# Performance work log

Hardware: AMD Instinct MI355X
Metric: run time of the kernel (lower is better)

The kernel has to match this reference:

```python
import jax, jax.numpy as jnp
import numpy as np

N_NODES = 50000
N_EDGES = 800000
F_IN = 128
F_OUT = 128
EPS_STD = 1e-5  # PyG StdAggregation epsilon


def setup_inputs() -> dict:
    key = jax.random.key(0)
    ks = jax.random.split(key, 8)
    x = jax.random.normal(ks[0], (N_NODES, F_IN), dtype=jnp.float32)
    edge_index = jax.random.randint(ks[1], (2, N_EDGES), 0, N_NODES, dtype=jnp.int64)
    s = 0.02
    # pre_nn: Linear(2*F_IN -> F_IN)
    W_pre = jax.random.normal(ks[2], (2 * F_IN, F_IN), dtype=jnp.float32) * s
    b_pre = jnp.zeros((F_IN,), dtype=jnp.float32)
    # post_nn: Linear((1 + 4 aggregators * 1 scaler) * F_IN -> F_OUT)
    W_post = jax.random.normal(ks[3], (5 * F_IN, F_OUT), dtype=jnp.float32) * s
    b_post = jnp.zeros((F_OUT,), dtype=jnp.float32)
    # final lin: Linear(F_OUT -> F_OUT)
    W_lin = jax.random.normal(ks[4], (F_OUT, F_OUT), dtype=jnp.float32) * s
    b_lin = jnp.zeros((F_OUT,), dtype=jnp.float32)
    return {"x": x, "W_pre": W_pre, "b_pre": b_pre, "W_post": W_post,
            "b_post": b_post, "W_lin": W_lin, "b_lin": b_lin,
            "edge_index": edge_index}


def _pna_forward(x, W_pre, b_pre, W_post, b_post, W_lin, b_lin, edge_index):
    N = x.shape[0]
    src = edge_index[0]  # x_j (source / neighbor)
    dst = edge_index[1]  # x_i (target / aggregation index)

    # per-edge message: Linear(cat(x_i, x_j))  [E, F_IN]
    h = jnp.concatenate([x[dst], x[src]], axis=-1) @ W_pre + b_pre

    ones = jnp.ones((h.shape[0],), dtype=h.dtype)
    deg = jax.ops.segment_sum(ones, dst, num_segments=N)          # in-degree [N]
    deg_c = jnp.maximum(deg, 1.0)[:, None]

    s1 = jax.ops.segment_sum(h, dst, num_segments=N)
    s2 = jax.ops.segment_sum(h * h, dst, num_segments=N)
    mean = s1 / deg_c
    var = jax.nn.relu(s2 / deg_c - mean * mean)
    std = jnp.sqrt(var + EPS_STD)

    has_nb = (deg > 0)[:, None]
    mx = jax.ops.segment_max(h, dst, num_segments=N)
    mn = jax.ops.segment_min(h, dst, num_segments=N)
    mx = jnp.where(has_nb, mx, 0.0)
    mn = jnp.where(has_nb, mn, 0.0)

    # aggregators in declared order: mean, max, min, std -> [N, 4*F_IN]
    agg = jnp.concatenate([mean, mx, mn, std], axis=-1)

    # 'linear' degree scaler: deg / avg_deg
    avg_deg = jnp.mean(deg)
    agg = agg * (deg[:, None] / avg_deg)

    out = jnp.concatenate([x, agg], axis=-1) @ W_post + b_post
    out = out @ W_lin + b_lin
    return jax.nn.relu(out)


def reference(x, W_pre, b_pre, W_post, b_post, W_lin, b_lin, edge_index):
    return _pna_forward(x, W_pre, b_pre, W_post, b_post, W_lin, b_lin, edge_index)
```

## Files before the change

kernel.cpp:

```cpp
#include <hip/hip_runtime.h>
#include <hip/hip_bf16.h>
#include <math.h>


typedef _Float16 f16;
typedef _Float16 f16x8 __attribute__((ext_vector_type(8)));
typedef _Float16 f16x2 __attribute__((ext_vector_type(2)));
typedef float    f32x4 __attribute__((ext_vector_type(4)));

__device__ __forceinline__ unsigned packh2(float a, float b) {
  union { unsigned u; f16x2 h; } x; x.h = (f16x2){(f16)a, (f16)b}; return x.u;
}
__device__ __forceinline__ float2 unpackh2(unsigned v) {
  union { unsigned u; f16x2 h; } x; x.u = v;
  return make_float2((float)x.h.x, (float)x.h.y);
}

template<int KTOT, int KO1, bool HASB, bool RELU, bool OUTF16>
__global__ __launch_bounds__(256) void gemm_reg_k(
    const f16* __restrict__ A1, const f16* __restrict__ A2,
    const f16* __restrict__ Wt, const float* __restrict__ bias,
    float* __restrict__ outF, f16* __restrict__ outH, int M, int ldOut)
{
  const int tid = threadIdx.x;
  const int l   = tid & 63;
  const int w   = tid >> 6;
  const int wr  = (w >> 1) * 32;
  const int wc  = (w & 1) * 64;
  const int li  = l & 15, kg = l >> 4;
  const int rowBase = blockIdx.x * 64;
  const int colBase = blockIdx.y * 128;
  constexpr int ld2 = (KTOT > KO1) ? (KTOT - KO1) : 1;

  int aOff[2], a2Off[2], bOff[4];
#pragma unroll
  for (int r = 0; r < 2; ++r) {
    int gr = rowBase + wr + r * 16 + li; if (gr > M - 1) gr = M - 1;
    aOff[r] = gr * KO1; a2Off[r] = gr * ld2;
  }
#pragma unroll
  for (int c = 0; c < 4; ++c) bOff[c] = (colBase + wc + c * 16 + li) * KTOT;

  f32x4 acc[2][4];
#pragma unroll
  for (int r = 0; r < 2; ++r)
#pragma unroll
    for (int c = 0; c < 4; ++c) acc[r][c] = (f32x4){0.f, 0.f, 0.f, 0.f};

  f16x8 aA[2], bA[4], aB[2], bB[4];
  auto lf = [&](int k0, f16x8 a[2], f16x8 b[4]) {
    int k = k0 + kg * 8;
    if (KO1 == KTOT || k0 < KO1) {
#pragma unroll
      for (int r = 0; r < 2; ++r) a[r] = *reinterpret_cast<const f16x8*>(A1 + aOff[r] + k);
    } else {
#pragma unroll
      for (int r = 0; r < 2; ++r) a[r] = *reinterpret_cast<const f16x8*>(A2 + a2Off[r] + (k - KO1));
    }
#pragma unroll
    for (int c = 0; c < 4; ++c) b[c] = *reinterpret_cast<const f16x8*>(Wt + bOff[c] + k);
  };

  lf(0, aA, bA);
  for (int k0 = 0; k0 < KTOT; k0 += 64) {
    lf(k0 + 32, aB, bB);
#pragma unroll
    for (int r = 0; r < 2; ++r)
#pragma unroll
      for (int c = 0; c < 4; ++c)
        acc[r][c] = __builtin_amdgcn_mfma_f32_16x16x32_f16(aA[r], bA[c], acc[r][c], 0, 0, 0);
    if (k0 + 64 < KTOT) lf(k0 + 64, aA, bA);
#pragma unroll
    for (int r = 0; r < 2; ++r)
#pragma unroll
      for (int c = 0; c < 4; ++c)
        acc[r][c] = __builtin_amdgcn_mfma_f32_16x16x32_f16(aB[r], bB[c], acc[r][c], 0, 0, 0);
  }

  float bv[4];
#pragma unroll
  for (int c = 0; c < 4; ++c) {
    int col = colBase + wc + c * 16 + li;
    bv[c] = (HASB && col < 128) ? bias[col] : 0.f;
  }

  if constexpr (OUTF16) {
    __shared__ __align__(16) f16 Ls[64][136];
#pragma unroll
    for (int c = 0; c < 4; ++c) {
      int col = wc + c * 16 + li;
#pragma unroll
      for (int r = 0; r < 2; ++r)
#pragma unroll
        for (int j = 0; j < 4; ++j) {
          float v = acc[r][c][j] + bv[c];
          if (RELU) v = fmaxf(v, 0.f);
          Ls[wr + r * 16 + kg * 4 + j][col] = (f16)v;
        }
    }
    __syncthreads();
#pragma unroll
    for (int i = 0; i < 4; ++i) {
      int s = tid + 256 * i;
      int rr = s >> 4, cc = (s & 15) * 8;
      int gr = rowBase + rr;
      if (gr < M)
        *reinterpret_cast<float4*>(&outH[(size_t)gr * ldOut + colBase + cc]) =
            *reinterpret_cast<const float4*>(&Ls[rr][cc]);
    }
  } else {
    __shared__ __align__(16) float Lf[64][132];
#pragma unroll
    for (int c = 0; c < 4; ++c) {
      int col = wc + c * 16 + li;
#pragma unroll
      for (int r = 0; r < 2; ++r)
#pragma unroll
        for (int j = 0; j < 4; ++j) {
          float v = acc[r][c][j] + bv[c];
          if (RELU) v = fmaxf(v, 0.f);
          Lf[wr + r * 16 + kg * 4 + j][col] = v;
        }
    }
    __syncthreads();
#pragma unroll
    for (int i = 0; i < 8; ++i) {
      int s = tid + 256 * i;
      int rr = s >> 5, cc = (s & 31) * 4;
      int gr = rowBase + rr;
      if (gr < M)
        *reinterpret_cast<float4*>(&outF[(size_t)gr * ldOut + colBase + cc]) =
            *reinterpret_cast<const float4*>(&Lf[rr][cc]);
    }
  }
}

__global__ void cvt_x_k(const float* __restrict__ x, f16* __restrict__ xf, int n) {
  int i = (blockIdx.x * 256 + threadIdx.x) * 4;
  if (i < n) {
    float4 v = *reinterpret_cast<const float4*>(&x[i]);
    xf[i] = (f16)v.x; xf[i + 1] = (f16)v.y; xf[i + 2] = (f16)v.z; xf[i + 3] = (f16)v.w;
  }
}

__global__ void prep_wpre_k(const float* __restrict__ W, f16* __restrict__ Wt) {
  int e = blockIdx.x * 256 + threadIdx.x;
  if (e < 256 * 128) {
    int n = e >> 7, k = e & 127;
    float v = (n < 128) ? W[(size_t)k * 128 + n] : W[(size_t)(128 + k) * 128 + (n - 128)];
    Wt[e] = (f16)v;
  }
}

__global__ void fold_w_k(const float* __restrict__ Wpost, const float* __restrict__ bpost,
                         const float* __restrict__ Wlin,  const float* __restrict__ blin,
                         f16* __restrict__ WtComb, float* __restrict__ bcomb) {
  int e = blockIdx.x * 256 + threadIdx.x;
  if (e < 640 * 128) {
    int n = e / 640, k = e - n * 640;
    float s = 0.f;
#pragma unroll 4
    for (int m = 0; m < 128; ++m) s += Wpost[(size_t)k * 128 + m] * Wlin[(size_t)m * 128 + n];
    WtComb[(size_t)n * 640 + k] = (f16)s;
  } else if (e < 640 * 128 + 128) {
    int n = e - 640 * 128;
    float s = blin[n];
#pragma unroll 4
    for (int m = 0; m < 128; ++m) s += bpost[m] * Wlin[(size_t)m * 128 + n];
    bcomb[n] = s;
  }
}

__global__ void zero_k(int* __restrict__ p, int n) {
  int i = blockIdx.x * 256 + threadIdx.x;
  if (i < n) p[i] = 0;
}

__global__ void count_k(const int* __restrict__ ei, int* __restrict__ deg, int E) {
  int e = blockIdx.x * 256 + threadIdx.x;
  if (e < E) atomicAdd(&deg[ei[E + e]], 1);
}

__device__ __forceinline__ int blockExclScan(int v, int* wtot) {
  int lane = threadIdx.x & 63, wid = threadIdx.x >> 6;
  int x = v;
#pragma unroll
  for (int d = 1; d < 64; d <<= 1) {
    int y = __shfl_up(x, d);
    if (lane >= d) x += y;
  }
  if (lane == 63) wtot[wid] = x;
  __syncthreads();
  if (threadIdx.x == 0) {
    int s = 0;
#pragma unroll
    for (int k = 0; k < 4; ++k) { int t = wtot[k]; wtot[k] = s; s += t; }
  }
  __syncthreads();
  return wtot[wid] + x - v;
}

__global__ __launch_bounds__(256) void scan1_k(const int* __restrict__ deg,
                                               int* __restrict__ offs,
                                               int* __restrict__ partials, int n) {
  __shared__ int wtot[4];
  int i = blockIdx.x * 256 + threadIdx.x;
  int v = (i < n) ? deg[i] : 0;
  int e = blockExclScan(v, wtot);
  if (i < n) offs[i] = e;
  if (threadIdx.x == 255) partials[blockIdx.x] = e + v;
}

__global__ __launch_bounds__(256) void scan2_k(int* __restrict__ partials, int nb) {
  __shared__ int wtot[4];
  int v = (threadIdx.x < nb) ? partials[threadIdx.x] : 0;
  int e = blockExclScan(v, wtot);
  if (threadIdx.x < nb) partials[threadIdx.x] = e;
}

__global__ void scan3_k(const int* __restrict__ partials, int* __restrict__ offs,
                        int* __restrict__ cur, int n, int E) {
  int i = blockIdx.x * 256 + threadIdx.x;
  if (i < n) {
    int v = offs[i] + partials[i >> 8];
    offs[i] = v; cur[i] = v;
  }
  if (i == 0) offs[n] = E;
}

__global__ void scatter_k(const int* __restrict__ ei, int* __restrict__ cursor,
                          int* __restrict__ ssrc, int E) {
  int e = blockIdx.x * 256 + threadIdx.x;
  if (e < E) {
    int d = ei[E + e];
    int pos = atomicAdd(&cursor[d], 1);
    ssrc[pos] = ei[e];
  }
}

__global__ __launch_bounds__(256) void agg_k(
    const f16* __restrict__ CP, const int* __restrict__ offs,
    const int* __restrict__ ssrc, f16* __restrict__ AGG, int N)
{
  int w = threadIdx.x >> 6;
  int t = threadIdx.x & 63;
  int i = blockIdx.x * 4 + w;
  if (i >= N) return;
  int start = offs[i], end = offs[i + 1];
  int deg = end - start;
  unsigned* AGGu = (unsigned*)AGG;
  size_t o = (size_t)i * 256 + t;
  if (deg == 0) {
    AGGu[o] = 0u; AGGu[o + 64] = 0u; AGGu[o + 128] = 0u; AGGu[o + 192] = 0u;
    return;
  }
  const unsigned* CPu = (const unsigned*)CP;
  float s0 = 0.f, s1 = 0.f, q0 = 0.f, q1 = 0.f;
  float mx0 = -INFINITY, mx1 = -INFINITY, mn0 = INFINITY, mn1 = INFINITY;

  auto accum = [&](unsigned u) {
    float2 v = unpackh2(u);
    s0 += v.x; s1 += v.y;
    q0 = fmaf(v.x, v.x, q0); q1 = fmaf(v.y, v.y, q1);
    mx0 = fmaxf(mx0, v.x); mx1 = fmaxf(mx1, v.y);
    mn0 = fminf(mn0, v.x); mn1 = fminf(mn1, v.y);
  };

  for (int base = start; base < end; base += 64) {
    int cnt = min(end - base, 64);
    int myoff = 0;
    if (base + t < end) myoff = ssrc[base + t] * 128 + 64;
    int j = 0;
    for (; j + 4 <= cnt; j += 4) {
      int o0 = __shfl(myoff, j);
      int o1 = __shfl(myoff, j + 1);
      int o2 = __shfl(myoff, j + 2);
      int o3 = __shfl(myoff, j + 3);
      unsigned u0 = CPu[o0 + t];
      unsigned u1 = CPu[o1 + t];
      unsigned u2 = CPu[o2 + t];
      unsigned u3 = CPu[o3 + t];
      accum(u0); accum(u1); accum(u2); accum(u3);
    }
    for (; j < cnt; ++j) {
      int o0 = __shfl(myoff, j);
      accum(CPu[o0 + t]);
    }
  }

  float2 c = unpackh2(CPu[(size_t)i * 128 + t]);
  float degf = (float)deg;
  float inv = 1.f / degf;
  float m10 = s0 * inv, m11 = s1 * inv;
  float var0 = fmaxf(q0 * inv - m10 * m10, 0.f);
  float var1 = fmaxf(q1 * inv - m11 * m11, 0.f);
  float sd0 = sqrtf(var0 + 1e-5f), sd1 = sqrtf(var1 + 1e-5f);
  float sc = degf * (1.0f / 16.0f);
  AGGu[o]       = packh2((c.x + m10) * sc, (c.y + m11) * sc);
  AGGu[o + 64]  = packh2((c.x + mx0) * sc, (c.y + mx1) * sc);
  AGGu[o + 128] = packh2((c.x + mn0) * sc, (c.y + mn1) * sc);
  AGGu[o + 192] = packh2(sd0 * sc, sd1 * sc);
}

extern "C" void kernel_launch(void* const* d_in, const int* in_sizes, int n_in,
                              void* d_out, int out_size, void* d_ws, size_t ws_size,
                              hipStream_t stream) {
  const float* x      = (const float*)d_in[0];
  const float* W_pre  = (const float*)d_in[1];
  const float* b_pre  = (const float*)d_in[2];
  const float* W_post = (const float*)d_in[3];
  const float* b_post = (const float*)d_in[4];
  const float* W_lin  = (const float*)d_in[5];
  const float* b_lin  = (const float*)d_in[6];
  const int*   ei     = (const int*)d_in[7];

  const int N = in_sizes[0] / 128;
  const int E = in_sizes[7] / 2;

  char* ws = (char*)d_ws;
  size_t off = 0;
  auto alloc = [&](size_t bytes) -> void* {
    void* p = ws + off; off += (bytes + 255) & ~(size_t)255; return p;
  };
  f16*   xf     = (f16*)  alloc((size_t)N * 128 * 2);
  f16*   CP     = (f16*)  alloc((size_t)N * 256 * 2);
  f16*   AGG    = (f16*)  alloc((size_t)N * 512 * 2);
  f16*   WtPre  = (f16*)  alloc(256 * 128 * 2);
  f16*   WtComb = (f16*)  alloc(128 * 640 * 2);
  float* bcomb  = (float*)alloc(128 * 4);
  int*   ssrc   = (int*)  alloc((size_t)E * 4);
  int*   deg    = (int*)  alloc((size_t)N * 4);
  int*   offs   = (int*)  alloc((size_t)(N + 1) * 4);
  int*   cur    = (int*)  alloc((size_t)N * 4);
  int*   parts  = (int*)  alloc(1024 * 4);

  const int gTile = (N + 63) / 64;
  const int gE    = (E + 255) / 256;
  const int gN    = (N + 255) / 256;

  cvt_x_k<<<(N * 128 / 4 + 255) / 256, 256, 0, stream>>>(x, xf, N * 128);
  prep_wpre_k<<<(256 * 128 + 255) / 256, 256, 0, stream>>>(W_pre, WtPre);
  fold_w_k<<<(640 * 128 + 128 + 255) / 256, 256, 0, stream>>>(W_post, b_post, W_lin, b_lin, WtComb, bcomb);

  zero_k<<<gN, 256, 0, stream>>>(deg, N);

  gemm_reg_k<128, 128, true, false, true><<<dim3(gTile, 2), 256, 0, stream>>>(
      xf, nullptr, WtPre, b_pre, nullptr, CP, N, 256);

  count_k<<<gE, 256, 0, stream>>>(ei, deg, E);
  scan1_k<<<gN, 256, 0, stream>>>(deg, offs, parts, N);
  scan2_k<<<1, 256, 0, stream>>>(parts, gN);
  scan3_k<<<gN, 256, 0, stream>>>(parts, offs, cur, N, E);
  scatter_k<<<gE, 256, 0, stream>>>(ei, cur, ssrc, E);

  agg_k<<<(N + 3) / 4, 256, 0, stream>>>(CP, offs, ssrc, AGG, N);

  gemm_reg_k<640, 128, true, true, false><<<dim3(gTile, 1), 256, 0, stream>>>(
      xf, AGG, WtComb, bcomb, (float*)d_out, nullptr, N, 128);
}
```

Before: 312.7 us.

## Fuse neighbor aggregation with post-GEMM via LDS, merge setup kernels

```diff
diff --git a/kernel.cpp b/kernel.cpp
--- a/kernel.cpp
+++ b/kernel.cpp
@@ -7,6 +7,8 @@
 typedef _Float16 f16x8 __attribute__((ext_vector_type(8)));
 typedef _Float16 f16x2 __attribute__((ext_vector_type(2)));
 typedef float    f32x4 __attribute__((ext_vector_type(4)));
+
+#define NPB 32
 
 __device__ __forceinline__ unsigned packh2(float a, float b) {
   union { unsigned u; f16x2 h; } x; x.h = (f16x2){(f16)a, (f16)b}; return x.u;
@@ -135,6 +137,141 @@
   }
 }
 
+__global__ __launch_bounds__(256) void aggmm_k(
+    const f16* __restrict__ CP, const f16* __restrict__ xf,
+    const int* __restrict__ offs, const int* __restrict__ ssrc,
+    const f16* __restrict__ Wt, const float* __restrict__ bcomb,
+    float* __restrict__ out, int N)
+{
+  __shared__ __align__(16) char ldsbuf[NPB * 1024];
+  const int tid = threadIdx.x;
+  const int l = tid & 63, w = tid >> 6;
+  const int blockBase = blockIdx.x * NPB;
+  const unsigned* CPu = (const unsigned*)CP;
+
+  {
+    const int t = l;
+    for (int q = 0; q < NPB / 4; ++q) {
+      const int rloc = w * (NPB / 4) + q;
+      const int i = blockBase + rloc;
+      const unsigned sw = ((unsigned)(rloc & 15)) << 4;
+      int deg = 0, start = 0;
+      if (i < N) { start = offs[i]; deg = offs[i + 1] - start; }
+      if (deg == 0) {
+        *reinterpret_cast<unsigned*>(&ldsbuf[rloc * 1024 + (((t)       * 4) ^ sw)]) = 0u;
+        *reinterpret_cast<unsigned*>(&ldsbuf[rloc * 1024 + (((t + 64)  * 4) ^ sw)]) = 0u;
+        *reinterpret_cast<unsigned*>(&ldsbuf[rloc * 1024 + (((t + 128) * 4) ^ sw)]) = 0u;
+        *reinterpret_cast<unsigned*>(&ldsbuf[rloc * 1024 + (((t + 192) * 4) ^ sw)]) = 0u;
+        continue;
+      }
+      const int end = start + deg;
+      float s0 = 0.f, s1 = 0.f, q0 = 0.f, q1 = 0.f;
+      float mx0 = -INFINITY, mx1 = -INFINITY, mn0 = INFINITY, mn1 = INFINITY;
+      auto accum = [&](unsigned u) {
+        float2 v = unpackh2(u);
+        s0 += v.x; s1 += v.y;
+        q0 = fmaf(v.x, v.x, q0); q1 = fmaf(v.y, v.y, q1);
+        mx0 = fmaxf(mx0, v.x); mx1 = fmaxf(mx1, v.y);
+        mn0 = fminf(mn0, v.x); mn1 = fminf(mn1, v.y);
+      };
+      for (int base = start; base < end; base += 64) {
+        int cnt = min(end - base, 64);
+        int myoff = 0;
+        if (base + t < end) myoff = ssrc[base + t] * 128 + 64;
+        int j = 0;
+        for (; j + 4 <= cnt; j += 4) {
+          int o0 = __shfl(myoff, j);
+          int o1 = __shfl(myoff, j + 1);
+          int o2 = __shfl(myoff, j + 2);
+          int o3 = __shfl(myoff, j + 3);
+          unsigned u0 = CPu[o0 + t];
+          unsigned u1 = CPu[o1 + t];
+          unsigned u2 = CPu[o2 + t];
+          unsigned u3 = CPu[o3 + t];
+          accum(u0); accum(u1); accum(u2); accum(u3);
+        }
+        for (; j < cnt; ++j) accum(CPu[__shfl(myoff, j) + t]);
+      }
+      float2 c = unpackh2(CPu[(size_t)i * 128 + t]);
+      float degf = (float)deg;
+      float inv = 1.f / degf;
+      float m10 = s0 * inv, m11 = s1 * inv;
+      float var0 = fmaxf(q0 * inv - m10 * m10, 0.f);
+      float var1 = fmaxf(q1 * inv - m11 * m11, 0.f);
+      float sd0 = sqrtf(var0 + 1e-5f), sd1 = sqrtf(var1 + 1e-5f);
+      float sc = degf * (1.0f / 16.0f);
+      *reinterpret_cast<unsigned*>(&ldsbuf[rloc * 1024 + (((t)       * 4) ^ sw)]) = packh2((c.x + m10) * sc, (c.y + m11) * sc);
+      *reinterpret_cast<unsigned*>(&ldsbuf[rloc * 1024 + (((t + 64)  * 4) ^ sw)]) = packh2((c.x + mx0) * sc, (c.y + mx1) * sc);
+      *reinterpret_cast<unsigned*>(&ldsbuf[rloc * 1024 + (((t + 128) * 4) ^ sw)]) = packh2((c.x + mn0) * sc, (c.y + mn1) * sc);
+      *reinterpret_cast<unsigned*>(&ldsbuf[rloc * 1024 + (((t + 192) * 4) ^ sw)]) = packh2(sd0 * sc, sd1 * sc);
+    }
+  }
+  __syncthreads();
+
+  const int li = l & 15, kg = l >> 4;
+  const int wr = (w >> 1) * 16;
+  const int wc = (w & 1) * 64;
+  const int aRow = wr + li;
+  int grA = blockBase + aRow; if (grA > N - 1) grA = N - 1;
+  const int aOffG = grA * 128;
+  const unsigned swA = ((unsigned)(aRow & 15)) << 4;
+  int bOff[4];
+#pragma unroll
+  for (int c = 0; c < 4; ++c) bOff[c] = (wc + c * 16 + li) * 640;
+
+  f32x4 acc[4];
+#pragma unroll
+  for (int c = 0; c < 4; ++c) acc[c] = (f32x4){0.f, 0.f, 0.f, 0.f};
+
+  auto lf = [&](int k0, f16x8& a, f16x8 b[4]) {
+    int k = k0 + kg * 8;
+    if (k0 < 128) {
+      a = *reinterpret_cast<const f16x8*>(xf + aOffG + k);
+    } else {
+      unsigned bo = (unsigned)((k - 128) * 2);
+      a = *reinterpret_cast<const f16x8*>(&ldsbuf[aRow * 1024 + (bo ^ swA)]);
+    }
+#pragma unroll
+    for (int c = 0; c < 4; ++c) b[c] = *reinterpret_cast<const f16x8*>(Wt + bOff[c] + k);
+  };
+  auto mm = [&](f16x8 a, f16x8 b[4]) {
+#pragma unroll
+    for (int c = 0; c < 4; ++c)
+      acc[c] = __builtin_amdgcn_mfma_f32_16x16x32_f16(a, b[c], acc[c], 0, 0, 0);
+  };
+
+  f16x8 aA, bA[4], aB, bB[4];
+  lf(0, aA, bA);
+  for (int k0 = 0; k0 < 640; k0 += 64) {
+    lf(k0 + 32, aB, bB);
+    mm(aA, bA);
+    if (k0 + 64 < 640) lf(k0 + 64, aA, bA);
+    mm(aB, bB);
+  }
+
+  float bv[4];
+#pragma unroll
+  for (int c = 0; c < 4; ++c) bv[c] = bcomb[wc + c * 16 + li];
+
+  __syncthreads();
+  float* Lf = (float*)ldsbuf;
+#pragma unroll
+  for (int c = 0; c < 4; ++c)
+#pragma unroll
+    for (int j = 0; j < 4; ++j)
+      Lf[(wr + kg * 4 + j) * 132 + wc + c * 16 + li] = fmaxf(acc[c][j] + bv[c], 0.f);
+  __syncthreads();
+#pragma unroll
+  for (int i2 = 0; i2 < 4; ++i2) {
+    int s = tid + 256 * i2;
+    int rr = s >> 5, cc = (s & 31) * 4;
+    int gr = blockBase + rr;
+    if (gr < N)
+      *reinterpret_cast<float4*>(&out[(size_t)gr * 128 + cc]) =
+          *reinterpret_cast<const float4*>(&Lf[rr * 132 + cc]);
+  }
+}
+
 __global__ void cvt_x_k(const float* __restrict__ x, f16* __restrict__ xf, int n) {
   int i = (blockIdx.x * 256 + threadIdx.x) * 4;
   if (i < n) {
@@ -143,37 +280,33 @@
   }
 }
 
-__global__ void prep_wpre_k(const float* __restrict__ W, f16* __restrict__ Wt) {
+__global__ void setup_k(const float* __restrict__ Wpre,
+                        const float* __restrict__ Wpost, const float* __restrict__ bpost,
+                        const float* __restrict__ Wlin,  const float* __restrict__ blin,
+                        f16* __restrict__ WtPre, f16* __restrict__ WtComb,
+                        float* __restrict__ bcomb, int* __restrict__ deg, int N) {
   int e = blockIdx.x * 256 + threadIdx.x;
   if (e < 256 * 128) {
     int n = e >> 7, k = e & 127;
-    float v = (n < 128) ? W[(size_t)k * 128 + n] : W[(size_t)(128 + k) * 128 + (n - 128)];
-    Wt[e] = (f16)v;
-  }
-}
-
-__global__ void fold_w_k(const float* __restrict__ Wpost, const float* __restrict__ bpost,
-                         const float* __restrict__ Wlin,  const float* __restrict__ blin,
-                         f16* __restrict__ WtComb, float* __restrict__ bcomb) {
-  int e = blockIdx.x * 256 + threadIdx.x;
-  if (e < 640 * 128) {
-    int n = e / 640, k = e - n * 640;
+    float v = (n < 128) ? Wpre[(size_t)k * 128 + n] : Wpre[(size_t)(128 + k) * 128 + (n - 128)];
+    WtPre[e] = (f16)v;
+  } else if (e < 256 * 128 + 640 * 128) {
+    int e2 = e - 256 * 128;
+    int n = e2 / 640, k = e2 - n * 640;
     float s = 0.f;
 #pragma unroll 4
     for (int m = 0; m < 128; ++m) s += Wpost[(size_t)k * 128 + m] * Wlin[(size_t)m * 128 + n];
     WtComb[(size_t)n * 640 + k] = (f16)s;
-  } else if (e < 640 * 128 + 128) {
-    int n = e - 640 * 128;
+  } else if (e < 256 * 128 + 640 * 128 + 128) {
+    int n = e - (256 * 128 + 640 * 128);
     float s = blin[n];
 #pragma unroll 4
     for (int m = 0; m < 128; ++m) s += bpost[m] * Wlin[(size_t)m * 128 + n];
     bcomb[n] = s;
-  }
-}
-
-__global__ void zero_k(int* __restrict__ p, int n) {
-  int i = blockIdx.x * 256 + threadIdx.x;
-  if (i < n) p[i] = 0;
+  } else {
+    int e3 = e - (256 * 128 + 640 * 128 + 128);
+    if (e3 < N) deg[e3] = 0;
+  }
 }
 
 __global__ void count_k(const int* __restrict__ ei, int* __restrict__ deg, int E) {
@@ -236,70 +369,6 @@
     int pos = atomicAdd(&cursor[d], 1);
     ssrc[pos] = ei[e];
   }
-}
-
-__global__ __launch_bounds__(256) void agg_k(
-    const f16* __restrict__ CP, const int* __restrict__ offs,
-    const int* __restrict__ ssrc, f16* __restrict__ AGG, int N)
-{
-  int w = threadIdx.x >> 6;
-  int t = threadIdx.x & 63;
-  int i = blockIdx.x * 4 + w;
-  if (i >= N) return;
-  int start = offs[i], end = offs[i + 1];
-  int deg = end - start;
-  unsigned* AGGu = (unsigned*)AGG;
-  size_t o = (size_t)i * 256 + t;
-  if (deg == 0) {
-    AGGu[o] = 0u; AGGu[o + 64] = 0u; AGGu[o + 128] = 0u; AGGu[o + 192] = 0u;
-    return;
-  }
-  const unsigned* CPu = (const unsigned*)CP;
-  float s0 = 0.f, s1 = 0.f, q0 = 0.f, q1 = 0.f;
-  float mx0 = -INFINITY, mx1 = -INFINITY, mn0 = INFINITY, mn1 = INFINITY;
-
-  auto accum = [&](unsigned u) {
-    float2 v = unpackh2(u);
-    s0 += v.x; s1 += v.y;
-    q0 = fmaf(v.x, v.x, q0); q1 = fmaf(v.y, v.y, q1);
-    mx0 = fmaxf(mx0, v.x); mx1 = fmaxf(mx1, v.y);
-    mn0 = fminf(mn0, v.x); mn1 = fminf(mn1, v.y);
-  };
-
-  for (int base = start; base < end; base += 64) {
-    int cnt = min(end - base, 64);
-    int myoff = 0;
-    if (base + t < end) myoff = ssrc[base + t] * 128 + 64;
-    int j = 0;
-    for (; j + 4 <= cnt; j += 4) {
-      int o0 = __shfl(myoff, j);
-      int o1 = __shfl(myoff, j + 1);
-      int o2 = __shfl(myoff, j + 2);
-      int o3 = __shfl(myoff, j + 3);
-      unsigned u0 = CPu[o0 + t];
-      unsigned u1 = CPu[o1 + t];
-      unsigned u2 = CPu[o2 + t];
-      unsigned u3 = CPu[o3 + t];
-      accum(u0); accum(u1); accum(u2); accum(u3);
-    }
-    for (; j < cnt; ++j) {
-      int o0 = __shfl(myoff, j);
-      accum(CPu[o0 + t]);
-    }
-  }
-
-  float2 c = unpackh2(CPu[(size_t)i * 128 + t]);
-  float degf = (float)deg;
-  float inv = 1.f / degf;
-  float m10 = s0 * inv, m11 = s1 * inv;
-  float var0 = fmaxf(q0 * inv - m10 * m10, 0.f);
-  float var1 = fmaxf(q1 * inv - m11 * m11, 0.f);
-  float sd0 = sqrtf(var0 + 1e-5f), sd1 = sqrtf(var1 + 1e-5f);
-  float sc = degf * (1.0f / 16.0f);
-  AGGu[o]       = packh2((c.x + m10) * sc, (c.y + m11) * sc);
-  AGGu[o + 64]  = packh2((c.x + mx0) * sc, (c.y + mx1) * sc);
-  AGGu[o + 128] = packh2((c.x + mn0) * sc, (c.y + mn1) * sc);
-  AGGu[o + 192] = packh2(sd0 * sc, sd1 * sc);
 }
 
 extern "C" void kernel_launch(void* const* d_in, const int* in_sizes, int n_in,
@@ -324,7 +393,6 @@
   };
   f16*   xf     = (f16*)  alloc((size_t)N * 128 * 2);
   f16*   CP     = (f16*)  alloc((size_t)N * 256 * 2);
-  f16*   AGG    = (f16*)  alloc((size_t)N * 512 * 2);
   f16*   WtPre  = (f16*)  alloc(256 * 128 * 2);
   f16*   WtComb = (f16*)  alloc(128 * 640 * 2);
   float* bcomb  = (float*)alloc(128 * 4);
@@ -335,14 +403,14 @@
   int*   parts  = (int*)  alloc(1024 * 4);
 
   const int gTile = (N + 63) / 64;
+  const int gFuse = (N + NPB - 1) / NPB;
   const int gE    = (E + 255) / 256;
   const int gN    = (N + 255) / 256;
+  const int setupElems = 256 * 128 + 640 * 128 + 128 + N;
 
   cvt_x_k<<<(N * 128 / 4 + 255) / 256, 256, 0, stream>>>(x, xf, N * 128);
-  prep_wpre_k<<<(256 * 128 + 255) / 256, 256, 0, stream>>>(W_pre, WtPre);
-  fold_w_k<<<(640 * 128 + 128 + 255) / 256, 256, 0, stream>>>(W_post, b_post, W_lin, b_lin, WtComb, bcomb);
-
-  zero_k<<<gN, 256, 0, stream>>>(deg, N);
+  setup_k<<<(setupElems + 255) / 256, 256, 0, stream>>>(W_pre, W_post, b_post, W_lin, b_lin,
+                                                        WtPre, WtComb, bcomb, deg, N);
 
   gemm_reg_k<128, 128, true, false, true><<<dim3(gTile, 2), 256, 0, stream>>>(
       xf, nullptr, WtPre, b_pre, nullptr, CP, N, 256);
@@ -353,8 +421,5 @@
   scan3_k<<<gN, 256, 0, stream>>>(parts, offs, cur, N, E);
   scatter_k<<<gE, 256, 0, stream>>>(ei, cur, ssrc, E);
 
-  agg_k<<<(N + 3) / 4, 256, 0, stream>>>(CP, offs, ssrc, AGG, N);
-
-  gemm_reg_k<640, 128, true, true, false><<<dim3(gTile, 1), 256, 0, stream>>>(
-      xf, AGG, WtComb, bcomb, (float*)d_out, nullptr, N, 128);
-}
+  aggmm_k<<<gFuse, 256, 0, stream>>>(CP, xf, offs, ssrc, WtComb, bcomb, (float*)d_out, N);
+}
```

Measured after the change: 362.6 us. 1.16x slower.
